# Kernel tuning notes

Hardware: AMD Instinct MI355X
Metric: run time of the kernel (lower is better)

## Reference

```python
import jax, jax.numpy as jnp
import numpy as np

T_GRID = 2048  # static grid size (= density * data range 128)
EPS = 1e-8


def rbf(x1, x2, ls, os_):
    # x1: [B,N,1], x2: [B,M,1] -> [B,N,M]; gpytorch ScaleKernel(RBFKernel())
    d2 = (x1 - jnp.swapaxes(x2, -1, -2)) ** 2
    return os_ * jnp.exp(-0.5 * d2 / (ls * ls))


def conv1d(x, w, b):
    # x: [B,C,T], w: [O,I,5], pad 2 -> same length
    y = jax.lax.conv_general_dilated(x, w, (1,), [(2, 2)],
                                     dimension_numbers=('NCH', 'OIH', 'NCH'))
    return y + b[None, :, None]


def setup_inputs() -> dict:
    key = jax.random.key(0)
    ks = jax.random.split(key, 12)
    B, Nc, Nt = 16, 2048, 2048
    xc = jax.random.uniform(ks[0], (B, Nc, 1), jnp.float32) * 128.0
    yc = jax.random.normal(ks[1], (B, Nc, 1), jnp.float32)
    xt = jax.random.uniform(ks[2], (B, Nt, 1), jnp.float32) * 128.0
    ln2 = float(np.log(2.0))  # softplus(0), gpytorch default raw param init
    params = {
        'ls_psi': jnp.float32(ln2), 'os_psi': jnp.float32(ln2),
        'ls_rho': jnp.float32(ln2), 'os_rho': jnp.float32(ln2),
        'w1': jax.random.normal(ks[3], (16, 3, 5), jnp.float32) * 0.2,
        'b1': jnp.zeros((16,), jnp.float32),
        'w2': jax.random.normal(ks[4], (32, 16, 5), jnp.float32) * 0.1,
        'b2': jnp.zeros((32,), jnp.float32),
        'w3': jax.random.normal(ks[5], (16, 32, 5), jnp.float32) * 0.1,
        'b3': jnp.zeros((16,), jnp.float32),
        'w4': jax.random.normal(ks[6], (2, 16, 5), jnp.float32) * 0.1,
        'b4': jnp.zeros((2,), jnp.float32),
    }
    return {'xc': xc, 'yc': yc, 'xt': xt, **params}


def reference(xc, yc, xt, ls_psi, os_psi, ls_rho, os_rho,
              w1, b1, w2, b2, w3, b3, w4, b4):
    B = xc.shape[0]
    lower = jnp.minimum(xc.min(), xt.min())
    upper = jnp.maximum(xc.max(), xt.max())
    t = jnp.linspace(lower, upper, T_GRID)                      # [T]
    t = jnp.broadcast_to(t[None, :, None], (B, T_GRID, 1))      # [B,T,1]

    # SetConv encoder: h = psi(t, xc) @ phi(yc), phi = [y^0, y^1]
    Kt = rbf(t, xc, ls_psi, os_psi)                             # [B,T,Nc]
    phi = jnp.concatenate([jnp.ones_like(yc), yc], -1)          # [B,Nc,2]
    h = jnp.matmul(Kt, phi)                                     # [B,T,2]
    h0, h1 = h[..., :1], h[..., 1:]
    h1 = h1 / (h0 + EPS)
    rep = jnp.concatenate([t, h0, h1], -1).swapaxes(-1, -2)     # [B,3,T]

    # small Conv1d decoder stack
    f = jax.nn.relu(conv1d(rep, w1, b1))
    f = jax.nn.relu(conv1d(f, w2, b2))
    f = jax.nn.relu(conv1d(f, w3, b3))
    f = conv1d(f, w4, b4).swapaxes(-1, -2)                      # [B,T,2]
    f_mu, f_sigma = f[..., :1], f[..., 1:]

    # SetConv decoder onto targets
    Kr = rbf(xt, t, ls_rho, os_rho)                             # [B,Nt,T]
    mu = jnp.matmul(Kr, f_mu)                                   # [B,Nt,1]
    sigma = jnp.matmul(Kr, jax.nn.softplus(f_sigma))            # [B,Nt,1]
    return jnp.concatenate([mu, sigma], -1)                     # [B,Nt,2]
```

## Files before the change

kernel.cpp:

```cpp
#include <hip/hip_runtime.h>
#include <math.h>

#define T_GRID 2048
#define NC 2048
#define NT 2048
#define BATCH 16
#define XCUT 28.0f
#define TILE 112
#define BW 133
#define PCAP 768
#define NSB 32

__global__ __launch_bounds__(1024) void k_minmax(const float4* __restrict__ xc4,
                                                 const float4* __restrict__ xt4,
                                                 float* __restrict__ mm) {
    float4 va[8], vb[8];
    int tid = threadIdx.x;
#pragma unroll
    for (int k = 0; k < 8; k++) va[k] = xc4[tid + 1024 * k];
#pragma unroll
    for (int k = 0; k < 8; k++) vb[k] = xt4[tid + 1024 * k];
    float lo = 3.4e38f, hi = -3.4e38f;
#pragma unroll
    for (int k = 0; k < 8; k++) {
        lo = fminf(lo, fminf(fminf(va[k].x, va[k].y), fminf(va[k].z, va[k].w)));
        hi = fmaxf(hi, fmaxf(fmaxf(va[k].x, va[k].y), fmaxf(va[k].z, va[k].w)));
        lo = fminf(lo, fminf(fminf(vb[k].x, vb[k].y), fminf(vb[k].z, vb[k].w)));
        hi = fmaxf(hi, fmaxf(fmaxf(vb[k].x, vb[k].y), fmaxf(vb[k].z, vb[k].w)));
    }
    for (int off = 32; off; off >>= 1) {
        lo = fminf(lo, __shfl_down(lo, off));
        hi = fmaxf(hi, __shfl_down(hi, off));
    }
    __shared__ float slo[16], shi[16];
    int lane = tid & 63, wv = tid >> 6;
    if (lane == 0) { slo[wv] = lo; shi[wv] = hi; }
    __syncthreads();
    if (tid == 0) {
        for (int w = 1; w < 16; w++) { lo = fminf(lo, slo[w]); hi = fmaxf(hi, shi[w]); }
        mm[0] = lo; mm[1] = hi;
    }
}

__global__ __launch_bounds__(512) void k_fused(
        const float* __restrict__ xc, const float* __restrict__ yc,
        const float* __restrict__ ls_psi, const float* __restrict__ os_psi,
        const float* __restrict__ mm,
        const float* __restrict__ w1, const float* __restrict__ b1,
        const float* __restrict__ w2, const float* __restrict__ b2,
        const float* __restrict__ w3, const float* __restrict__ b3,
        const float* __restrict__ w4, const float* __restrict__ b4,
        float* __restrict__ f) {
    __shared__ float rep[3][BW];
    __shared__ float L1s[16][BW];
    __shared__ __align__(16) char pool[32 * BW * 4];
    __shared__ float w1L[15][16];
    __shared__ float w2L[80][32];
    __shared__ float w3L[160][16];
    __shared__ float w4L[80][2];
    __shared__ float bL[66];

    float (*L2s)[BW] = reinterpret_cast<float (*)[BW]>(pool);
    float (*L3s)[BW] = L1s;
    float*  px     = reinterpret_cast<float*>(pool);
    float*  py     = reinterpret_cast<float*>(pool + 3072);
    float2* part   = reinterpret_cast<float2*>(pool + 6144);
    int*    bstart = reinterpret_cast<int*>(pool + 10240);
    int*    curi   = reinterpret_cast<int*>(pool + 10376);

    int tid = threadIdx.x;
    int b = blockIdx.y;
    int gstart = blockIdx.x * TILE - 8;

    for (int idx = tid; idx < 240; idx += 512)  { int o = idx / 15,  r2 = idx % 15;  w1L[r2][o] = w1[idx]; }
    for (int idx = tid; idx < 2560; idx += 512) { int o = idx / 80,  r2 = idx % 80;  w2L[r2][o] = w2[idx]; }
    for (int idx = tid; idx < 2560; idx += 512) { int o = idx / 160, r2 = idx % 160; w3L[r2][o] = w3[idx]; }
    for (int idx = tid; idx < 160; idx += 512)  { int o = idx / 80,  r2 = idx % 80;  w4L[r2][o] = w4[idx]; }
    if (tid < 16) bL[tid] = b1[tid];
    if (tid < 32) bL[16 + tid] = b2[tid];
    if (tid < 16) bL[48 + tid] = b3[tid];
    if (tid < 2)  bL[64 + tid] = b4[tid];
    if (tid < 4) {
        int c = (tid < 2) ? tid : tid + 128;
        for (int r2 = 0; r2 < 3; r2++)  rep[r2][c] = 0.f;
        for (int r2 = 0; r2 < 16; r2++) L1s[r2][c] = 0.f;
    }

    float lower = mm[0], upper = mm[1];
    float step = (upper - lower) * (1.0f / (T_GRID - 1));
    float ls = ls_psi[0], os = os_psi[0];
    float c2 = -0.72134752044f / (ls * ls);
    float R = ls * sqrtf(XCUT);

    int g0 = max(gstart, 0), g1 = min(gstart + 127, T_GRID - 1);
    float tmin = fmaf((float)g0, step, lower) - R;
    float tmax = fmaf((float)g1, step, lower) + R;
    float sbw_inv = (float)NSB / (tmax - tmin);

    if (tid < NSB + 1) bstart[tid] = 0;
    __syncthreads();
    float xv[4], yv[4];
    int bn[4];
    const float* xb = xc + b * NC;
    const float* yb = yc + b * NC;
#pragma unroll
    for (int k = 0; k < 4; k++) {
        int idx = tid + 512 * k;
        xv[k] = xb[idx];
        yv[k] = yb[idx];
        bool in = (xv[k] >= tmin) & (xv[k] <= tmax);
        bn[k] = -1;
        if (in) {
            bn[k] = min(NSB - 1, max(0, (int)((xv[k] - tmin) * sbw_inv)));
            atomicAdd(&bstart[bn[k]], 1);
        }
    }
    __syncthreads();
    if (tid == 0) {
        int run = 0;
        for (int i = 0; i < NSB; i++) { int c = bstart[i]; bstart[i] = run; run += c; }
        bstart[NSB] = run;
    }
    __syncthreads();
    if (tid < NSB) curi[tid] = bstart[tid];
    __syncthreads();
#pragma unroll
    for (int k = 0; k < 4; k++) {
        if (bn[k] >= 0) {
            int pos = atomicAdd(&curi[bn[k]], 1);
            if (pos < PCAP) { px[pos] = xv[k]; py[pos] = yv[k]; }
        }
    }
    __syncthreads();

    {
        int p = tid & 127, rr = tid >> 7;
        int gp = gstart + p;
        bool pvalid = (gp >= 0 && gp < T_GRID);
        float t = fmaf((float)gp, step, lower);
        int s = 0, e = 0;
        if (pvalid) {
            int b0 = min(NSB - 1, max(0, (int)((t - R - tmin) * sbw_inv)));
            int b1 = min(NSB - 1, max(0, (int)((t + R - tmin) * sbw_inv)));
            s = bstart[b0];
            e = min(bstart[b1 + 1], PCAP);
        }
        float S0 = 0.f, S1 = 0.f;
        for (int j = s + rr; j < e; j += 4) {
            float xj = px[j], yj = py[j];
            float d = t - xj;
            float ev = exp2f(d * d * c2);
            S0 += ev;
            S1 = fmaf(ev, yj, S1);
        }
        part[tid] = make_float2(S0, S1);
        __syncthreads();
        if (tid < 128) {
            float2 q1 = part[tid + 128], q2 = part[tid + 256], q3 = part[tid + 384];
            S0 += q1.x + q2.x + q3.x;
            S1 += q1.y + q2.y + q3.y;
            float h0 = os * S0;
            float h1 = os * S1 / (h0 + 1e-8f);
            rep[0][p + 2] = pvalid ? t : 0.f;
            rep[1][p + 2] = pvalid ? h0 : 0.f;
            rep[2][p + 2] = pvalid ? h1 : 0.f;
        }
    }
    __syncthreads();

    {
        if (tid < 4) {
            int c = (tid < 2) ? tid : tid + 128;
            for (int r2 = 0; r2 < 32; r2++) L2s[r2][c] = 0.f;
        }
        int o = tid & 15, s0 = (tid >> 4) << 2;
        float acc[4];
        float bias = bL[o];
#pragma unroll
        for (int s = 0; s < 4; s++) acc[s] = bias;
        for (int i = 0; i < 3; i++) {
            float x[8];
#pragma unroll
            for (int j = 0; j < 8; j++) x[j] = rep[i][s0 + j];
#pragma unroll
            for (int k = 0; k < 5; k++) {
                float w = w1L[i * 5 + k][o];
#pragma unroll
                for (int s = 0; s < 4; s++) acc[s] = fmaf(x[s + k], w, acc[s]);
            }
        }
#pragma unroll
        for (int s = 0; s < 4; s++) {
            int p = s0 + s, gp = gstart + p;
            bool vv = (p >= 2 && p < 126 && gp >= 0 && gp < T_GRID);
            L1s[o][p + 2] = vv ? fmaxf(acc[s], 0.f) : 0.f;
        }
    }
    __syncthreads();

    {
        int o = tid & 31, s0 = (tid >> 5) << 3;
        float acc[8];
        float bias = bL[16 + o];
#pragma unroll
        for (int s = 0; s < 8; s++) acc[s] = bias;
        for (int i = 0; i < 16; i++) {
            float x[12];
#pragma unroll
            for (int j = 0; j < 12; j++) x[j] = L1s[i][s0 + j];
#pragma unroll
            for (int k = 0; k < 5; k++) {
                float w = w2L[i * 5 + k][o];
#pragma unroll
                for (int s = 0; s < 8; s++) acc[s] = fmaf(x[s + k], w, acc[s]);
            }
        }
#pragma unroll
        for (int s = 0; s < 8; s++) {
            int p = s0 + s, gp = gstart + p;
            bool vv = (p >= 4 && p < 124 && gp >= 0 && gp < T_GRID);
            L2s[o][p + 2] = vv ? fmaxf(acc[s], 0.f) : 0.f;
        }
    }
    __syncthreads();

    {
        int o = tid & 15, s0 = (tid >> 4) << 2;
        float acc[4];
        float bias = bL[48 + o];
#pragma unroll
        for (int s = 0; s < 4; s++) acc[s] = bias;
        for (int i = 0; i < 32; i++) {
            float x[8];
#pragma unroll
            for (int j = 0; j < 8; j++) x[j] = L2s[i][s0 + j];
#pragma unroll
            for (int k = 0; k < 5; k++) {
                float w = w3L[i * 5 + k][o];
#pragma unroll
                for (int s = 0; s < 4; s++) acc[s] = fmaf(x[s + k], w, acc[s]);
            }
        }
        __syncthreads();
#pragma unroll
        for (int s = 0; s < 4; s++) {
            int p = s0 + s, gp = gstart + p;
            bool vv = (p >= 6 && p < 122 && gp >= 0 && gp < T_GRID);
            L3s[o][p + 2] = vv ? fmaxf(acc[s], 0.f) : 0.f;
        }
    }
    __syncthreads();

    if (tid < 256) {
        int o = tid & 1, p = tid >> 1;
        float a = bL[64 + o];
        for (int i = 0; i < 16; i++) {
#pragma unroll
            for (int k = 0; k < 5; k++) {
                a = fmaf(L3s[i][p + k], w4L[i * 5 + k][o], a);
            }
        }
        int gp = gstart + p;
        if (p >= 8 && p < 120 && gp >= 0 && gp < T_GRID) {
            if (o) {
                float sp = fmaxf(a, 0.f) + log1pf(expf(-fabsf(a)));
                f[2 * (b * T_GRID + gp) + 1] = sp;
            } else {
                f[2 * (b * T_GRID + gp)] = a;
            }
        }
    }
}

__global__ __launch_bounds__(256) void k_out(const float* __restrict__ xt,
                                             const float* __restrict__ ls_rho,
                                             const float* __restrict__ os_rho,
                                             const float* __restrict__ mm,
                                             const float2* __restrict__ f,
                                             float2* __restrict__ out) {
    __shared__ float smx[T_GRID];
    __shared__ float ssg[T_GRID];
    __shared__ float2 part[256];
    int b = blockIdx.y, tid = threadIdx.x;
    int it = blockIdx.x * 64 + (tid & 63);
    int r = tid >> 6;
    float lower = mm[0], upper = mm[1];
    float step = (upper - lower) * (1.0f / (T_GRID - 1));
    float invstep = 1.0f / step;
    float ls = ls_rho[0], os = os_rho[0];
    float c2 = -0.72134752044f / (ls * ls);
    float R = ls * sqrtf(XCUT);
    float x = xt[b * NT + it];

    const float2* fb = f + b * T_GRID;
    for (int k = tid; k < T_GRID; k += 256) {
        float2 v = fb[k];
        smx[k] = v.x; ssg[k] = v.y;
    }
    __syncthreads();

    int j0 = max(0, (int)floorf((x - R - lower) * invstep));
    int j1 = min(T_GRID - 1, (int)ceilf((x + R - lower) * invstep));

    float Smu = 0.f, Ssg = 0.f;
    float jf = (float)(j0 + r);
    for (int j = j0 + r; j <= j1; j += 4) {
        float d = x - fmaf(jf, step, lower);
        float e = exp2f(d * d * c2);
        Smu = fmaf(e, smx[j], Smu);
        Ssg = fmaf(e, ssg[j], Ssg);
        jf += 4.0f;
    }
    part[tid] = make_float2(Smu, Ssg);
    __syncthreads();
    if (r == 0) {
#pragma unroll
        for (int q = 64; q < 256; q += 64) {
            float2 pp = part[tid + q];
            Smu += pp.x; Ssg += pp.y;
        }
        out[b * NT + it] = make_float2(os * Smu, os * Ssg);
    }
}

extern "C" void kernel_launch(void* const* d_in, const int* in_sizes, int n_in,
                              void* d_out, int out_size, void* d_ws, size_t ws_size,
                              hipStream_t stream) {
    const float* xc = (const float*)d_in[0];
    const float* yc = (const float*)d_in[1];
    const float* xt = (const float*)d_in[2];
    const float* ls_psi = (const float*)d_in[3];
    const float* os_psi = (const float*)d_in[4];
    const float* ls_rho = (const float*)d_in[5];
    const float* os_rho = (const float*)d_in[6];
    const float* w1 = (const float*)d_in[7];
    const float* b1 = (const float*)d_in[8];
    const float* w2 = (const float*)d_in[9];
    const float* b2 = (const float*)d_in[10];
    const float* w3 = (const float*)d_in[11];
    const float* b3 = (const float*)d_in[12];
    const float* w4 = (const float*)d_in[13];
    const float* b4 = (const float*)d_in[14];

    char* ws = (char*)d_ws;
    float* mm = (float*)ws;
    float* f  = (float*)(ws + 64);

    k_minmax<<<dim3(1), dim3(1024), 0, stream>>>((const float4*)xc, (const float4*)xt, mm);

    int ntiles = (T_GRID + TILE - 1) / TILE;
    k_fused<<<dim3(ntiles, BATCH), dim3(512), 0, stream>>>(
        xc, yc, ls_psi, os_psi, mm,
        w1, b1, w2, b2, w3, b3, w4, b4, f);

    k_out<<<dim3(NT / 64, BATCH), dim3(256), 0, stream>>>(
        xt, ls_rho, os_rho, mm, (const float2*)f, (float2*)d_out);
}
```

Measured before the change: 113.0 us.

## Widen fused conv tile to 128 outputs with 144-wide halo and 576 threads

```diff
diff --git a/kernel.cpp b/kernel.cpp
--- a/kernel.cpp
+++ b/kernel.cpp
@@ -6,8 +6,9 @@
 #define NT 2048
 #define BATCH 16
 #define XCUT 28.0f
-#define TILE 112
-#define BW 133
+#define TILE 128
+#define SW 144
+#define W 149
 #define PCAP 768
 #define NSB 32
 
@@ -42,7 +43,7 @@
     }
 }
 
-__global__ __launch_bounds__(512) void k_fused(
+__global__ __launch_bounds__(576) void k_fused(
         const float* __restrict__ xc, const float* __restrict__ yc,
         const float* __restrict__ ls_psi, const float* __restrict__ os_psi,
         const float* __restrict__ mm,
@@ -51,37 +52,37 @@
         const float* __restrict__ w3, const float* __restrict__ b3,
         const float* __restrict__ w4, const float* __restrict__ b4,
         float* __restrict__ f) {
-    __shared__ float rep[3][BW];
-    __shared__ float L1s[16][BW];
-    __shared__ __align__(16) char pool[32 * BW * 4];
+    __shared__ float rep[3][W];
+    __shared__ float L1s[16][W];
+    __shared__ __align__(16) char pool[32 * W * 4];
     __shared__ float w1L[15][16];
     __shared__ float w2L[80][32];
     __shared__ float w3L[160][16];
     __shared__ float w4L[80][2];
     __shared__ float bL[66];
 
-    float (*L2s)[BW] = reinterpret_cast<float (*)[BW]>(pool);
-    float (*L3s)[BW] = L1s;
+    float (*L2s)[W] = reinterpret_cast<float (*)[W]>(pool);
+    float (*L3s)[W] = L1s;
     float*  px     = reinterpret_cast<float*>(pool);
     float*  py     = reinterpret_cast<float*>(pool + 3072);
     float2* part   = reinterpret_cast<float2*>(pool + 6144);
-    int*    bstart = reinterpret_cast<int*>(pool + 10240);
-    int*    curi   = reinterpret_cast<int*>(pool + 10376);
+    int*    bstart = reinterpret_cast<int*>(pool + 10752);
+    int*    curi   = reinterpret_cast<int*>(pool + 10896);
 
     int tid = threadIdx.x;
     int b = blockIdx.y;
     int gstart = blockIdx.x * TILE - 8;
 
-    for (int idx = tid; idx < 240; idx += 512)  { int o = idx / 15,  r2 = idx % 15;  w1L[r2][o] = w1[idx]; }
-    for (int idx = tid; idx < 2560; idx += 512) { int o = idx / 80,  r2 = idx % 80;  w2L[r2][o] = w2[idx]; }
-    for (int idx = tid; idx < 2560; idx += 512) { int o = idx / 160, r2 = idx % 160; w3L[r2][o] = w3[idx]; }
-    for (int idx = tid; idx < 160; idx += 512)  { int o = idx / 80,  r2 = idx % 80;  w4L[r2][o] = w4[idx]; }
+    for (int idx = tid; idx < 240; idx += 576)  { int o = idx / 15,  r2 = idx % 15;  w1L[r2][o] = w1[idx]; }
+    for (int idx = tid; idx < 2560; idx += 576) { int o = idx / 80,  r2 = idx % 80;  w2L[r2][o] = w2[idx]; }
+    for (int idx = tid; idx < 2560; idx += 576) { int o = idx / 160, r2 = idx % 160; w3L[r2][o] = w3[idx]; }
+    for (int idx = tid; idx < 160; idx += 576)  { int o = idx / 80,  r2 = idx % 80;  w4L[r2][o] = w4[idx]; }
     if (tid < 16) bL[tid] = b1[tid];
     if (tid < 32) bL[16 + tid] = b2[tid];
     if (tid < 16) bL[48 + tid] = b3[tid];
     if (tid < 2)  bL[64 + tid] = b4[tid];
     if (tid < 4) {
-        int c = (tid < 2) ? tid : tid + 128;
+        int c = (tid < 2) ? tid : tid + SW;
         for (int r2 = 0; r2 < 3; r2++)  rep[r2][c] = 0.f;
         for (int r2 = 0; r2 < 16; r2++) L1s[r2][c] = 0.f;
     }
@@ -92,7 +93,7 @@
     float c2 = -0.72134752044f / (ls * ls);
     float R = ls * sqrtf(XCUT);
 
-    int g0 = max(gstart, 0), g1 = min(gstart + 127, T_GRID - 1);
+    int g0 = max(gstart, 0), g1 = min(gstart + SW - 1, T_GRID - 1);
     float tmin = fmaf((float)g0, step, lower) - R;
     float tmax = fmaf((float)g1, step, lower) + R;
     float sbw_inv = (float)NSB / (tmax - tmin);
@@ -105,14 +106,15 @@
     const float* yb = yc + b * NC;
 #pragma unroll
     for (int k = 0; k < 4; k++) {
-        int idx = tid + 512 * k;
-        xv[k] = xb[idx];
-        yv[k] = yb[idx];
-        bool in = (xv[k] >= tmin) & (xv[k] <= tmax);
+        int idx = tid + 576 * k;
         bn[k] = -1;
-        if (in) {
-            bn[k] = min(NSB - 1, max(0, (int)((xv[k] - tmin) * sbw_inv)));
-            atomicAdd(&bstart[bn[k]], 1);
+        if (idx < NC) {
+            xv[k] = xb[idx];
+            yv[k] = yb[idx];
+            if ((xv[k] >= tmin) & (xv[k] <= tmax)) {
+                bn[k] = min(NSB - 1, max(0, (int)((xv[k] - tmin) * sbw_inv)));
+                atomicAdd(&bstart[bn[k]], 1);
+            }
         }
     }
     __syncthreads();
@@ -134,7 +136,7 @@
     __syncthreads();
 
     {
-        int p = tid & 127, rr = tid >> 7;
+        int p = tid >> 2, rr = tid & 3;
         int gp = gstart + p;
         bool pvalid = (gp >= 0 && gp < T_GRID);
         float t = fmaf((float)gp, step, lower);
@@ -153,24 +155,26 @@
             S0 += ev;
             S1 = fmaf(ev, yj, S1);
         }
-        part[tid] = make_float2(S0, S1);
+        part[rr * SW + p] = make_float2(S0, S1);
         __syncthreads();
-        if (tid < 128) {
-            float2 q1 = part[tid + 128], q2 = part[tid + 256], q3 = part[tid + 384];
-            S0 += q1.x + q2.x + q3.x;
-            S1 += q1.y + q2.y + q3.y;
-            float h0 = os * S0;
-            float h1 = os * S1 / (h0 + 1e-8f);
-            rep[0][p + 2] = pvalid ? t : 0.f;
-            rep[1][p + 2] = pvalid ? h0 : 0.f;
-            rep[2][p + 2] = pvalid ? h1 : 0.f;
+        if (tid < SW) {
+            float2 q0 = part[tid], q1 = part[tid + SW], q2 = part[tid + 2 * SW], q3 = part[tid + 3 * SW];
+            float T0 = q0.x + q1.x + q2.x + q3.x;
+            float T1 = q0.y + q1.y + q2.y + q3.y;
+            int gp2 = gstart + tid;
+            bool pv2 = (gp2 >= 0 && gp2 < T_GRID);
+            float h0 = os * T0;
+            float h1 = os * T1 / (h0 + 1e-8f);
+            rep[0][tid + 2] = pv2 ? fmaf((float)gp2, step, lower) : 0.f;
+            rep[1][tid + 2] = pv2 ? h0 : 0.f;
+            rep[2][tid + 2] = pv2 ? h1 : 0.f;
         }
     }
     __syncthreads();
 
     {
         if (tid < 4) {
-            int c = (tid < 2) ? tid : tid + 128;
+            int c = (tid < 2) ? tid : tid + SW;
             for (int r2 = 0; r2 < 32; r2++) L2s[r2][c] = 0.f;
         }
         int o = tid & 15, s0 = (tid >> 4) << 2;
@@ -192,7 +196,7 @@
 #pragma unroll
         for (int s = 0; s < 4; s++) {
             int p = s0 + s, gp = gstart + p;
-            bool vv = (p >= 2 && p < 126 && gp >= 0 && gp < T_GRID);
+            bool vv = (p >= 2 && p < SW - 2 && gp >= 0 && gp < T_GRID);
             L1s[o][p + 2] = vv ? fmaxf(acc[s], 0.f) : 0.f;
         }
     }
@@ -218,7 +222,7 @@
 #pragma unroll
         for (int s = 0; s < 8; s++) {
             int p = s0 + s, gp = gstart + p;
-            bool vv = (p >= 4 && p < 124 && gp >= 0 && gp < T_GRID);
+            bool vv = (p >= 4 && p < SW - 4 && gp >= 0 && gp < T_GRID);
             L2s[o][p + 2] = vv ? fmaxf(acc[s], 0.f) : 0.f;
         }
     }
@@ -241,33 +245,30 @@
                 for (int s = 0; s < 4; s++) acc[s] = fmaf(x[s + k], w, acc[s]);
             }
         }
-        __syncthreads();
 #pragma unroll
         for (int s = 0; s < 4; s++) {
             int p = s0 + s, gp = gstart + p;
-            bool vv = (p >= 6 && p < 122 && gp >= 0 && gp < T_GRID);
+            bool vv = (p >= 6 && p < SW - 6 && gp >= 0 && gp < T_GRID);
             L3s[o][p + 2] = vv ? fmaxf(acc[s], 0.f) : 0.f;
         }
     }
     __syncthreads();
 
     if (tid < 256) {
-        int o = tid & 1, p = tid >> 1;
+        int o = tid & 1, po = tid >> 1;
         float a = bL[64 + o];
         for (int i = 0; i < 16; i++) {
 #pragma unroll
             for (int k = 0; k < 5; k++) {
-                a = fmaf(L3s[i][p + k], w4L[i * 5 + k][o], a);
-            }
-        }
-        int gp = gstart + p;
-        if (p >= 8 && p < 120 && gp >= 0 && gp < T_GRID) {
-            if (o) {
-                float sp = fmaxf(a, 0.f) + log1pf(expf(-fabsf(a)));
-                f[2 * (b * T_GRID + gp) + 1] = sp;
-            } else {
-                f[2 * (b * T_GRID + gp)] = a;
-            }
+                a = fmaf(L3s[i][po + 8 + k], w4L[i * 5 + k][o], a);
+            }
+        }
+        int gp = blockIdx.x * TILE + po;
+        if (o) {
+            float sp = fmaxf(a, 0.f) + log1pf(expf(-fabsf(a)));
+            f[2 * (b * T_GRID + gp) + 1] = sp;
+        } else {
+            f[2 * (b * T_GRID + gp)] = a;
         }
     }
 }
@@ -348,8 +349,7 @@
 
     k_minmax<<<dim3(1), dim3(1024), 0, stream>>>((const float4*)xc, (const float4*)xt, mm);
 
-    int ntiles = (T_GRID + TILE - 1) / TILE;
-    k_fused<<<dim3(ntiles, BATCH), dim3(512), 0, stream>>>(
+    k_fused<<<dim3(T_GRID / TILE, BATCH), dim3(576), 0, stream>>>(
         xc, yc, ls_psi, os_psi, mm,
         w1, b1, w2, b2, w3, b3, w4, b4, f);
 
```

Result: faster. 109.6 us (-3.0%).
